# Kernel optimization log

Hardware: AMD Instinct MI355X
Metric: run time of the kernel (lower is better)

## Reference

```python
import jax, jax.numpy as jnp
import numpy as np

# seek_thermal sensor constants (hard-coded in the torch module)
HFOV, VFOV = 81.0, 59.0
H, W = 150, 200
P = 1024   # max_num_points
M = 5      # max_num_persons


def _cam_grids():
    fx = W / (2.0 * np.tan(np.deg2rad(HFOV) / 2.0))
    fy = H / (2.0 * np.tan(np.deg2rad(VFOV) / 2.0))
    x, y = np.meshgrid(np.arange(W), np.arange(H))
    x_cam = (x - W / 2.0) / fx
    y_cam = (y - H / 2.0) / fy
    return jnp.asarray(x_cam, jnp.float32), jnp.asarray(y_cam, jnp.float32)


def setup_inputs() -> dict:
    key = jax.random.key(0)
    k1, k2, k3 = jax.random.split(key, 3)
    B = 256
    depth = jax.random.uniform(k1, (B, H, W), jnp.float32, 0.0, 12.0)
    ind = jax.random.randint(k2, (B, H, W), 0, M + 1).astype(jnp.float32)
    extra = jax.random.normal(k3, (B, H, W), dtype=jnp.float32)
    return {"depth_mask_3C": jnp.stack([depth, ind, extra], axis=1)}


def _percentile(d_sorted, n, q):
    # np.percentile 'linear' interpolation on ascending sorted valid depths
    nf = n.astype(d_sorted.dtype)
    pos = q * jnp.maximum(nf - 1.0, 0.0)
    lo = jnp.floor(pos).astype(jnp.int32)
    hi = jnp.ceil(pos).astype(jnp.int32)
    frac = pos - lo.astype(d_sorted.dtype)
    return d_sorted[lo] * (1.0 - frac) + d_sorted[hi] * frac


def _person(depth, ind, x_cam, y_cam, p):
    # depth, ind: (H, W); p: scalar person id (float)
    mask = (ind == p) & (depth > 3.0)
    n = mask.sum()
    # invalid pixels pushed to +inf so the first n sorted entries are the valid depths
    d_sorted = jnp.sort(jnp.where(mask, depth, jnp.inf).reshape(-1))
    q1 = _percentile(d_sorted, n, 0.25)
    q3 = _percentile(d_sorted, n, 0.75)
    iqr = q3 - q1
    lb = q1 - 1.5 * iqr
    ub = q3 + 1.5 * iqr
    mask2 = (mask & (depth >= lb) & (depth <= ub)).reshape(-1)  # (H*W,)
    pts = jnp.stack(
        [(x_cam * depth).reshape(-1), (y_cam * depth).reshape(-1), depth.reshape(-1)],
        axis=-1,
    )  # (H*W, 3)
    # deterministic compaction: first max_num_points surviving pixels in raster order
    rank = jnp.cumsum(mask2.astype(jnp.int32)) - 1
    write_idx = jnp.where(mask2 & (rank < P), rank, P)  # slot P is a dump slot
    buf = jnp.zeros((P + 1, 3), depth.dtype).at[write_idx].set(
        jnp.where(mask2[:, None], pts, 0.0)
    )
    flag = mask2.any().astype(depth.dtype)
    flag_col = jnp.zeros((3,), depth.dtype).at[0].set(flag)
    return jnp.concatenate([buf[:P].T, flag_col[:, None]], axis=1)  # (3, P+1)


def reference(depth_mask_3C):
    x_cam, y_cam = _cam_grids()
    depth = depth_mask_3C[:, 0]
    ind = jnp.round(depth_mask_3C[:, 1])
    persons = jnp.arange(1, M + 1, dtype=depth.dtype)
    per_b = jax.vmap(_person, in_axes=(None, None, None, None, 0))
    res = jax.vmap(per_b, in_axes=(0, 0, None, None, None))(
        depth, ind, x_cam, y_cam, persons
    )  # (B, M, 3, P+1)
    B = depth.shape[0]
    return res.transpose(0, 2, 1, 3).reshape(B, 3, M * (P + 1))
```

## Files before the change

### kernel.cpp

```cpp
#include <hip/hip_runtime.h>
#include <math.h>

#define HW_N   30000
#define NV4    7500
#define W_IMG  200
#define H_IMG  150
#define NPERS  5
#define CAP    1024
#define NTHR   1024
#define NWAVE  16
#define CAPS   384
#define NREG   (NWAVE * NPERS)
#define BASE_BITS 0x40400000u

#ifndef M_PI
#define M_PI 3.14159265358979323846
#endif

__device__ __forceinline__ unsigned wave_incl_scan_u32(unsigned v, int lane) {
    #pragma unroll
    for (int d = 1; d < 64; d <<= 1) {
        unsigned t = __shfl_up(v, d, 64);
        if (lane >= d) v += t;
    }
    return v;
}

__device__ __forceinline__ void find_bucket(const unsigned* h, int nchunks, unsigned k,
                                            int lane, unsigned& bucket, unsigned& cl) {
    unsigned run = 0;
    bucket = 0; cl = 0;
    bool found = false;
    for (int c = 0; c < nchunks; ++c) {
        if (found) break;
        unsigned hv = h[c * 64 + lane] & 0xFFFFu;
        unsigned inc = wave_incl_scan_u32(hv, lane);
        unsigned tot = __shfl(inc, 63, 64);
        if (run + tot > k) {
            unsigned long long m = __ballot((run + inc) > k);
            int l = (int)__builtin_ctzll(m);
            bucket = (unsigned)(c * 64 + l);
            cl = run + __shfl(inc, l, 64) - __shfl(hv, l, 64);
            found = true;
        }
        run += tot;
    }
}

__device__ __forceinline__ int person_of(float f) {
    float r = rintf(f);
    int p = (int)r;
    return (p >= 1 && p <= NPERS && (float)p == r) ? p : 0;
}

extern "C" __global__ __launch_bounds__(NTHR)
void DepthMask2PointCloudFast_53472342835417_kernel(const float* __restrict__ in,
                                                    float* __restrict__ out) {
    const int b = blockIdx.x;
    const int tid = (int)threadIdx.x;
    const int lane = tid & 63;
    const int wv = tid >> 6;

    const float* __restrict__ depth = in + (size_t)b * 3u * HW_N;
    const float* __restrict__ indc = depth + HW_N;
    const float4* __restrict__ d4p = (const float4*)depth;
    const float4* __restrict__ i4p = (const float4*)indc;

    __shared__ unsigned s_vals[NREG * CAPS];
    __shared__ unsigned s_cur[NREG];
    __shared__ unsigned s_h1[NPERS * 256];
    __shared__ unsigned s_h2[20 * 256];
    __shared__ __align__(16) unsigned s_pref[24];
    __shared__ int      s_krem[20];
    __shared__ float    s_val[20];
    __shared__ unsigned s_n[NPERS];
    __shared__ float    s_lb[NPERS], s_ub[NPERS];
    __shared__ unsigned s_cnt[NWAVE][NPERS];
    __shared__ unsigned s_woff[NWAVE][NPERS];
    __shared__ unsigned s_tot[NPERS];
    __shared__ unsigned s_base[NPERS];
    __shared__ float    s_xc[W_IMG];
    __shared__ float    s_yc[H_IMG];

    for (int i = tid; i < NPERS * 256; i += NTHR) s_h1[i] = 0u;
    for (int i = tid; i < 20 * 256; i += NTHR) s_h2[i] = 0u;
    if (tid < NREG) s_cur[tid] = 0u;
    if (tid < NPERS) { s_base[tid] = 0u; s_tot[tid] = 0u; }
    if (tid < W_IMG) {
        const double fx = 200.0 / (2.0 * tan((81.0 * (M_PI / 180.0)) / 2.0));
        s_xc[tid] = (float)(((double)tid - 100.0) / fx);
    }
    {
        int ty = tid - 256;
        if (ty >= 0 && ty < H_IMG) {
            const double fy = 150.0 / (2.0 * tan((59.0 * (M_PI / 180.0)) / 2.0));
            s_yc[ty] = (float)(((double)ty - 75.0) / fy);
        }
    }
    __syncthreads();

    {
        int i = tid;
        float4 dd = d4p[i], ff = i4p[i];
        while (i < NV4) {
            int inx = i + NTHR;
            float4 dd2, ff2;
            if (inx < NV4) { dd2 = d4p[inx]; ff2 = i4p[inx]; }
            float de[4] = {dd.x, dd.y, dd.z, dd.w};
            float fe[4] = {ff.x, ff.y, ff.z, ff.w};
            #pragma unroll
            for (int e = 0; e < 4; ++e) {
                float d = de[e];
                int p = person_of(fe[e]);
                if (p && d > 3.0f) {
                    unsigned k24 = __float_as_uint(d) - BASE_BITS;
                    atomicAdd(&s_h1[(p - 1) * 256 + (k24 >> 16)], 1u);
                    int reg = wv * NPERS + (p - 1);
                    unsigned off = atomicAdd(&s_cur[reg], 1u);
                    if (off < CAPS) s_vals[reg * CAPS + off] = k24;
                }
            }
            dd = dd2; ff = ff2;
            i = inx;
        }
    }
    __syncthreads();

    if (tid < NPERS) {
        unsigned n = 0;
        for (int sh = 0; sh < NWAVE; ++sh) n += s_cur[sh * NPERS + tid];
        s_n[tid] = n;
    }
    __syncthreads();

    for (int q = wv; q < 20; q += NWAVE) {
        int p = q >> 2, s = q & 3;
        unsigned n = s_n[p];
        if (n == 0u) { if (lane == 0) s_pref[q] = 0xFFFFFFFFu; continue; }
        float nf = (float)n;
        float m1 = fmaxf(nf - 1.0f, 0.0f);
        float pos = ((s >> 1) ? 0.75f : 0.25f) * m1;
        unsigned k = (unsigned)((s & 1) ? (int)ceilf(pos) : (int)floorf(pos));
        unsigned bucket, cl;
        find_bucket(&s_h1[p * 256], 4, k, lane, bucket, cl);
        if (lane == 0) { s_pref[q] = bucket; s_krem[q] = (int)(k - cl); }
    }
    __syncthreads();

    for (int t = tid; t < NREG * CAPS; t += NTHR) {
        int reg = t / CAPS;
        int ii = t - reg * CAPS;
        unsigned cnt = s_cur[reg]; if (cnt > CAPS) cnt = CAPS;
        if ((unsigned)ii < cnt) {
            unsigned k24 = s_vals[t];
            int p = reg % NPERS;
            unsigned t8 = k24 >> 16;
            uint4 pr = *(const uint4*)&s_pref[p * 4];
            unsigned b8 = (k24 >> 8) & 255u;
            if (t8 == pr.x) atomicAdd(&s_h2[(p * 4 + 0) * 256 + b8], 1u);
            if (t8 == pr.y) atomicAdd(&s_h2[(p * 4 + 1) * 256 + b8], 1u);
            if (t8 == pr.z) atomicAdd(&s_h2[(p * 4 + 2) * 256 + b8], 1u);
            if (t8 == pr.w) atomicAdd(&s_h2[(p * 4 + 3) * 256 + b8], 1u);
        }
    }
    __syncthreads();

    for (int q = wv; q < 20; q += NWAVE) {
        int p = q >> 2;
        if (s_n[p] == 0u) continue;
        unsigned bucket, cl;
        find_bucket(&s_h2[q * 256], 4, (unsigned)s_krem[q], lane, bucket, cl);
        if (lane == 0) { s_pref[q] = (s_pref[q] << 8) | bucket; s_krem[q] -= (int)cl; }
    }
    __syncthreads();
    for (int i = tid; i < 20 * 256; i += NTHR) s_h2[i] = 0u;
    __syncthreads();

    for (int t = tid; t < NREG * CAPS; t += NTHR) {
        int reg = t / CAPS;
        int ii = t - reg * CAPS;
        unsigned cnt = s_cur[reg]; if (cnt > CAPS) cnt = CAPS;
        if ((unsigned)ii < cnt) {
            unsigned k24 = s_vals[t];
            int p = reg % NPERS;
            unsigned t16 = k24 >> 8;
            uint4 pr = *(const uint4*)&s_pref[p * 4];
            unsigned b8 = k24 & 255u;
            if (t16 == pr.x) atomicAdd(&s_h2[(p * 4 + 0) * 256 + b8], 1u);
            if (t16 == pr.y) atomicAdd(&s_h2[(p * 4 + 1) * 256 + b8], 1u);
            if (t16 == pr.z) atomicAdd(&s_h2[(p * 4 + 2) * 256 + b8], 1u);
            if (t16 == pr.w) atomicAdd(&s_h2[(p * 4 + 3) * 256 + b8], 1u);
        }
    }
    __syncthreads();

    for (int q = wv; q < 20; q += NWAVE) {
        int p = q >> 2;
        if (s_n[p] == 0u) continue;
        unsigned bucket, cl;
        find_bucket(&s_h2[q * 256], 4, (unsigned)s_krem[q], lane, bucket, cl);
        if (lane == 0) s_val[q] = __uint_as_float(BASE_BITS + ((s_pref[q] << 8) | bucket));
    }
    __syncthreads();

    if (tid < NPERS) {
        if (s_n[tid] == 0u) {
            s_lb[tid] = INFINITY; s_ub[tid] = -INFINITY;
        } else {
            float nf = (float)s_n[tid];
            float m1 = fmaxf(nf - 1.0f, 0.0f);
            float pos1 = 0.25f * m1, pos3 = 0.75f * m1;
            float fr1 = pos1 - floorf(pos1);
            float fr3 = pos3 - floorf(pos3);
            float q1 = __fadd_rn(__fmul_rn(s_val[tid * 4 + 0], __fsub_rn(1.0f, fr1)),
                                 __fmul_rn(s_val[tid * 4 + 1], fr1));
            float q3 = __fadd_rn(__fmul_rn(s_val[tid * 4 + 2], __fsub_rn(1.0f, fr3)),
                                 __fmul_rn(s_val[tid * 4 + 3], fr3));
            float iqr = __fsub_rn(q3, q1);
            float t15 = __fmul_rn(1.5f, iqr);
            s_lb[tid] = __fsub_rn(q1, t15);
            s_ub[tid] = __fadd_rn(q3, t15);
        }
    }
    __syncthreads();

    float* outb = out + (size_t)b * 3u * (NPERS * (CAP + 1));
    const int cstr = NPERS * (CAP + 1);

    for (int t0 = 0; t0 < NV4; t0 += NTHR) {
        int i = t0 + tid;
        int pf[4] = {0, 0, 0, 0};
        float dv[4] = {0.f, 0.f, 0.f, 0.f};
        if (i < NV4) {
            float4 dd = d4p[i];
            float4 ff = i4p[i];
            float de[4] = {dd.x, dd.y, dd.z, dd.w};
            float fe[4] = {ff.x, ff.y, ff.z, ff.w};
            #pragma unroll
            for (int e = 0; e < 4; ++e) {
                float d = de[e];
                int p = person_of(fe[e]);
                dv[e] = d;
                if (p && d > 3.0f && d >= s_lb[p - 1] && d <= s_ub[p - 1]) pf[e] = p;
            }
        }
        unsigned wexc[NPERS];
        #pragma unroll
        for (int pp = 0; pp < NPERS; ++pp) {
            unsigned c = (unsigned)((pf[0] == pp + 1) + (pf[1] == pp + 1) +
                                    (pf[2] == pp + 1) + (pf[3] == pp + 1));
            unsigned incl = wave_incl_scan_u32(c, lane);
            if (lane == 63) s_cnt[wv][pp] = incl;
            wexc[pp] = incl - c;
        }
        __syncthreads();
        if (tid < 16 * NPERS) {
            int p = tid >> 4, w = tid & 15;
            unsigned o = s_base[p];
            for (int w2 = 0; w2 < w; ++w2) o += s_cnt[w2][p];
            s_woff[w][p] = o;
            if (w == 15) s_tot[p] = o + s_cnt[15][p];
        }
        __syncthreads();
        #pragma unroll
        for (int pp = 0; pp < NPERS; ++pp) {
            unsigned m0 = (pf[0] == pp + 1), m1 = (pf[1] == pp + 1);
            unsigned m2 = (pf[2] == pp + 1), m3 = (pf[3] == pp + 1);
            if ((m0 | m1 | m2 | m3) != 0u) {
                unsigned basep = s_woff[wv][pp] + wexc[pp];
                #define WRITEPT(e, mm, pre)                                                \
                    if (mm) { unsigned off = basep + (pre);                                \
                        if (off < CAP) {                                                   \
                            int idx = i * 4 + e; int y = idx / W_IMG; int x = idx - y * W_IMG; \
                            size_t o = (size_t)pp * (CAP + 1) + off; float d = dv[e];      \
                            outb[o] = __fmul_rn(s_xc[x], d);                               \
                            outb[cstr + o] = __fmul_rn(s_yc[y], d);                        \
                            outb[2 * cstr + o] = d; } }
                WRITEPT(0, m0, 0u)
                WRITEPT(1, m1, m0)
                WRITEPT(2, m2, m0 + m1)
                WRITEPT(3, m3, m0 + m1 + m2)
                #undef WRITEPT
            }
        }
        if (tid < NPERS) s_base[tid] = s_tot[tid];
        bool done = true;
        #pragma unroll
        for (int pp = 0; pp < NPERS; ++pp) done = done && (s_tot[pp] >= (unsigned)CAP);
        if (done) break;
    }
    __syncthreads();

    for (int t = tid; t < NPERS * (CAP + 1); t += NTHR) {
        int p = t / (CAP + 1);
        int j = t - p * (CAP + 1);
        unsigned cnt = s_tot[p];
        size_t o = (size_t)p * (CAP + 1) + j;
        if (j == CAP) {
            outb[o] = (cnt > 0u) ? 1.0f : 0.0f;
            outb[cstr + o] = 0.0f;
            outb[2 * cstr + o] = 0.0f;
        } else if ((unsigned)j >= cnt) {
            outb[o] = 0.0f;
            outb[cstr + o] = 0.0f;
            outb[2 * cstr + o] = 0.0f;
        }
    }
}

extern "C" void kernel_launch(void* const* d_in, const int* in_sizes, int n_in,
                              void* d_out, int out_size, void* d_ws, size_t ws_size,
                              hipStream_t stream) {
    const float* in = (const float*)d_in[0];
    float* out = (float*)d_out;
    int B = in_sizes[0] / (3 * HW_N);
    hipLaunchKernelGGL(DepthMask2PointCloudFast_53472342835417_kernel,
                       dim3(B), dim3(NTHR), 0, stream, in, out);
}
```

Measured before the change: 52.95 us.

## Split per-image kernel into capture, select and output kernels via workspace

```diff
diff --git a/kernel.cpp b/kernel.cpp
--- a/kernel.cpp
+++ b/kernel.cpp
@@ -7,11 +7,8 @@
 #define H_IMG  150
 #define NPERS  5
 #define CAP    1024
-#define NTHR   1024
-#define NWAVE  16
-#define CAPS   384
-#define NREG   (NWAVE * NPERS)
 #define BASE_BITS 0x40400000u
+#define VCAP   4096
 
 #ifndef M_PI
 #define M_PI 3.14159265358979323846
@@ -26,8 +23,284 @@
     return v;
 }
 
-__device__ __forceinline__ void find_bucket(const unsigned* h, int nchunks, unsigned k,
-                                            int lane, unsigned& bucket, unsigned& cl) {
+__device__ __forceinline__ int person_of(float f) {
+    float r = rintf(f);
+    int p = (int)r;
+    return (p >= 1 && p <= NPERS && (float)p == r) ? p : 0;
+}
+
+__device__ __forceinline__ void sel256(const unsigned* h, unsigned k, int lane,
+                                       unsigned& bucket, unsigned& krem) {
+    unsigned run = 0; bucket = 0; krem = 0;
+    bool found = false;
+    #pragma unroll
+    for (int c = 0; c < 4; ++c) {
+        if (found) continue;
+        unsigned hv = h[c * 64 + lane];
+        unsigned inc = wave_incl_scan_u32(hv, lane);
+        unsigned tot = __shfl(inc, 63, 64);
+        if (run + tot > k) {
+            unsigned long long m = __ballot((run + inc) > k);
+            int l = (int)__builtin_ctzll(m);
+            bucket = (unsigned)(c * 64 + l);
+            krem = k - (run + __shfl(inc, l, 64) - __shfl(hv, l, 64));
+            found = true;
+        } else run += tot;
+    }
+}
+
+__global__ __launch_bounds__(256)
+void k1_capture(const float* __restrict__ in, unsigned* __restrict__ vals,
+                unsigned* __restrict__ cnt) {
+    const int bid = blockIdx.x;
+    const int b = bid >> 2, s = bid & 3;
+    const int tid = (int)threadIdx.x, lane = tid & 63;
+    const float* __restrict__ depth = in + (size_t)b * 3u * HW_N;
+    const float4* __restrict__ d4p = (const float4*)depth;
+    const float4* __restrict__ i4p = (const float4*)(depth + HW_N);
+    const int f40 = s * (NV4 / 4), f41 = f40 + (NV4 / 4);
+
+    for (int base4 = f40; base4 < f41; base4 += 256) {
+        int i = base4 + tid;
+        bool valid = i < f41;
+        float4 dd, ff;
+        if (valid) { dd = d4p[i]; ff = i4p[i]; }
+        int pf[4] = {0, 0, 0, 0};
+        unsigned kk[4] = {0, 0, 0, 0};
+        if (valid) {
+            float de[4] = {dd.x, dd.y, dd.z, dd.w};
+            float fe[4] = {ff.x, ff.y, ff.z, ff.w};
+            #pragma unroll
+            for (int e = 0; e < 4; ++e) {
+                float d = de[e];
+                int p = person_of(fe[e]);
+                if (p && d > 3.0f) { pf[e] = p; kk[e] = __float_as_uint(d) - BASE_BITS; }
+            }
+        }
+        #pragma unroll
+        for (int pp = 1; pp <= NPERS; ++pp) {
+            unsigned m0 = (pf[0] == pp), m1 = (pf[1] == pp);
+            unsigned m2 = (pf[2] == pp), m3 = (pf[3] == pp);
+            unsigned c = m0 + m1 + m2 + m3;
+            unsigned incl = wave_incl_scan_u32(c, lane);
+            unsigned tot = __shfl(incl, 63, 64);
+            if (tot == 0u) continue;
+            unsigned base = 0u;
+            if (lane == 0) base = atomicAdd(&cnt[b * NPERS + pp - 1], tot);
+            base = (unsigned)__shfl((int)base, 0, 64);
+            unsigned wexc = incl - c;
+            unsigned* vp = vals + (size_t)(b * NPERS + pp - 1) * VCAP;
+            unsigned o = base + wexc;
+            if (m0 && o < VCAP) vp[o] = kk[0];
+            o += m0;
+            if (m1 && o < VCAP) vp[o] = kk[1];
+            o += m1;
+            if (m2 && o < VCAP) vp[o] = kk[2];
+            o += m2;
+            if (m3 && o < VCAP) vp[o] = kk[3];
+        }
+    }
+}
+
+__global__ __launch_bounds__(256)
+void k2_select(const unsigned* __restrict__ vals, const unsigned* __restrict__ cnt,
+               float* __restrict__ bounds) {
+    const int bp = blockIdx.x;
+    const int tid = (int)threadIdx.x, lane = tid & 63, wv = tid >> 6;
+
+    __shared__ unsigned s_v[VCAP];
+    __shared__ unsigned s_h1[256];
+    __shared__ unsigned s_h2[4 * 256];
+    __shared__ unsigned s_pref[4];
+    __shared__ unsigned s_krem[4];
+    __shared__ float    s_val[4];
+
+    unsigned n = cnt[bp];
+    if (n == 0u) {
+        if (tid == 0) { bounds[bp * 2] = INFINITY; bounds[bp * 2 + 1] = -INFINITY; }
+        return;
+    }
+    unsigned nn = n > VCAP ? VCAP : n;
+    s_h1[tid] = 0u;
+    #pragma unroll
+    for (int j = 0; j < 4; ++j) s_h2[j * 256 + tid] = 0u;
+    __syncthreads();
+
+    const unsigned* vsrc = vals + (size_t)bp * VCAP;
+    for (int i = tid; i < (int)nn; i += 256) {
+        unsigned v = vsrc[i];
+        s_v[i] = v;
+        atomicAdd(&s_h1[v >> 16], 1u);
+    }
+    __syncthreads();
+
+    {
+        float nf = (float)n;
+        float m1 = fmaxf(nf - 1.0f, 0.0f);
+        float pos = ((wv >> 1) ? 0.75f : 0.25f) * m1;
+        unsigned k = (unsigned)((wv & 1) ? (int)ceilf(pos) : (int)floorf(pos));
+        unsigned bucket, krem;
+        sel256(s_h1, k, lane, bucket, krem);
+        if (lane == 0) { s_pref[wv] = bucket; s_krem[wv] = krem; }
+    }
+    __syncthreads();
+
+    {
+        unsigned p0 = s_pref[0], p1 = s_pref[1], p2 = s_pref[2], p3 = s_pref[3];
+        for (int i = tid; i < (int)nn; i += 256) {
+            unsigned v = s_v[i];
+            unsigned t8 = v >> 16, b8 = (v >> 8) & 255u;
+            if (t8 == p0) atomicAdd(&s_h2[b8], 1u);
+            if (t8 == p1) atomicAdd(&s_h2[256 + b8], 1u);
+            if (t8 == p2) atomicAdd(&s_h2[512 + b8], 1u);
+            if (t8 == p3) atomicAdd(&s_h2[768 + b8], 1u);
+        }
+    }
+    __syncthreads();
+    {
+        unsigned bucket, krem;
+        sel256(&s_h2[wv * 256], s_krem[wv], lane, bucket, krem);
+        if (lane == 0) { s_pref[wv] = (s_pref[wv] << 8) | bucket; s_krem[wv] = krem; }
+    }
+    __syncthreads();
+    #pragma unroll
+    for (int j = 0; j < 4; ++j) s_h2[j * 256 + tid] = 0u;
+    __syncthreads();
+
+    {
+        unsigned p0 = s_pref[0], p1 = s_pref[1], p2 = s_pref[2], p3 = s_pref[3];
+        for (int i = tid; i < (int)nn; i += 256) {
+            unsigned v = s_v[i];
+            unsigned t16 = v >> 8, b8 = v & 255u;
+            if (t16 == p0) atomicAdd(&s_h2[b8], 1u);
+            if (t16 == p1) atomicAdd(&s_h2[256 + b8], 1u);
+            if (t16 == p2) atomicAdd(&s_h2[512 + b8], 1u);
+            if (t16 == p3) atomicAdd(&s_h2[768 + b8], 1u);
+        }
+    }
+    __syncthreads();
+    {
+        unsigned bucket, krem;
+        sel256(&s_h2[wv * 256], s_krem[wv], lane, bucket, krem);
+        if (lane == 0) s_val[wv] = __uint_as_float(BASE_BITS + ((s_pref[wv] << 8) | bucket));
+    }
+    __syncthreads();
+
+    if (tid == 0) {
+        float nf = (float)n;
+        float m1 = fmaxf(nf - 1.0f, 0.0f);
+        float pos1 = 0.25f * m1, pos3 = 0.75f * m1;
+        float fr1 = pos1 - floorf(pos1);
+        float fr3 = pos3 - floorf(pos3);
+        float q1 = __fadd_rn(__fmul_rn(s_val[0], __fsub_rn(1.0f, fr1)),
+                             __fmul_rn(s_val[1], fr1));
+        float q3 = __fadd_rn(__fmul_rn(s_val[2], __fsub_rn(1.0f, fr3)),
+                             __fmul_rn(s_val[3], fr3));
+        float iqr = __fsub_rn(q3, q1);
+        float t15 = __fmul_rn(1.5f, iqr);
+        bounds[bp * 2]     = __fsub_rn(q1, t15);
+        bounds[bp * 2 + 1] = __fadd_rn(q3, t15);
+    }
+}
+
+__global__ __launch_bounds__(256)
+void k3_output(const float* __restrict__ in, const float* __restrict__ bounds,
+               float* __restrict__ out) {
+    const int bp = blockIdx.x;
+    const int b = bp / NPERS, p = bp % NPERS;
+    const int tid = (int)threadIdx.x, lane = tid & 63, wv = tid >> 6;
+    const int ptgt = p + 1;
+
+    __shared__ float s_xc[W_IMG], s_yc[H_IMG];
+    __shared__ unsigned s_wcnt[4], s_woff[4];
+    __shared__ unsigned s_gbase;
+
+    if (tid < W_IMG) {
+        const double fx = 200.0 / (2.0 * tan((81.0 * (M_PI / 180.0)) / 2.0));
+        s_xc[tid] = (float)(((double)tid - 100.0) / fx);
+    }
+    if (tid < H_IMG) {
+        const double fy = 150.0 / (2.0 * tan((59.0 * (M_PI / 180.0)) / 2.0));
+        s_yc[tid] = (float)(((double)tid - 75.0) / fy);
+    }
+    if (tid == 0) s_gbase = 0u;
+
+    const float lb = bounds[bp * 2], ub = bounds[bp * 2 + 1];
+    const float* __restrict__ depth = in + (size_t)b * 3u * HW_N;
+    const float4* __restrict__ d4p = (const float4*)depth;
+    const float4* __restrict__ i4p = (const float4*)(depth + HW_N);
+    float* r0 = out + (size_t)b * 3u * (NPERS * (CAP + 1)) + (size_t)p * (CAP + 1);
+    const int cstr = NPERS * (CAP + 1);
+    __syncthreads();
+
+    for (int base4 = 0; base4 < NV4; base4 += 256) {
+        int i = base4 + tid;
+        bool valid = i < NV4;
+        float4 dd, ff;
+        if (valid) { dd = d4p[i]; ff = i4p[i]; }
+        unsigned m[4] = {0, 0, 0, 0};
+        float dv[4] = {0.f, 0.f, 0.f, 0.f};
+        if (valid) {
+            float de[4] = {dd.x, dd.y, dd.z, dd.w};
+            float fe[4] = {ff.x, ff.y, ff.z, ff.w};
+            #pragma unroll
+            for (int e = 0; e < 4; ++e) {
+                float d = de[e];
+                dv[e] = d;
+                if (person_of(fe[e]) == ptgt && d > 3.0f && d >= lb && d <= ub) m[e] = 1u;
+            }
+        }
+        unsigned c = m[0] + m[1] + m[2] + m[3];
+        unsigned incl = wave_incl_scan_u32(c, lane);
+        if (lane == 63) s_wcnt[wv] = incl;
+        unsigned wexc = incl - c;
+        __syncthreads();
+        if (tid == 0) {
+            unsigned o = s_gbase;
+            #pragma unroll
+            for (int w = 0; w < 4; ++w) { s_woff[w] = o; o += s_wcnt[w]; }
+            s_gbase = o;
+        }
+        __syncthreads();
+        if (c) {
+            unsigned o = s_woff[wv] + wexc;
+            #pragma unroll
+            for (int e = 0; e < 4; ++e) {
+                if (m[e]) {
+                    if (o < CAP) {
+                        int idx = i * 4 + e;
+                        int y = idx / W_IMG, x = idx - y * W_IMG;
+                        float d = dv[e];
+                        r0[o]            = __fmul_rn(s_xc[x], d);
+                        r0[cstr + o]     = __fmul_rn(s_yc[y], d);
+                        r0[2 * cstr + o] = d;
+                    }
+                    ++o;
+                }
+            }
+        }
+        if (s_gbase >= (unsigned)CAP) break;
+    }
+    __syncthreads();
+    unsigned cntv = s_gbase;
+    unsigned cl = cntv > (unsigned)CAP ? (unsigned)CAP : cntv;
+    for (int j = (int)cl + tid; j < CAP; j += 256) {
+        r0[j] = 0.0f; r0[cstr + j] = 0.0f; r0[2 * cstr + j] = 0.0f;
+    }
+    if (tid == 0) {
+        r0[CAP] = (cntv > 0u) ? 1.0f : 0.0f;
+        r0[cstr + CAP] = 0.0f;
+        r0[2 * cstr + CAP] = 0.0f;
+    }
+}
+
+#define NTHR 1024
+#define NWAVE 16
+#define CAPS 384
+#define NREG (NWAVE * NPERS)
+
+__device__ __forceinline__ void find_bucket_fb(const unsigned* h, int nchunks, unsigned k,
+                                               int lane, unsigned& bucket, unsigned& cl) {
     unsigned run = 0;
     bucket = 0; cl = 0;
     bool found = false;
@@ -47,20 +320,12 @@
     }
 }
 
-__device__ __forceinline__ int person_of(float f) {
-    float r = rintf(f);
-    int p = (int)r;
-    return (p >= 1 && p <= NPERS && (float)p == r) ? p : 0;
-}
-
-extern "C" __global__ __launch_bounds__(NTHR)
-void DepthMask2PointCloudFast_53472342835417_kernel(const float* __restrict__ in,
-                                                    float* __restrict__ out) {
+__global__ __launch_bounds__(NTHR)
+void fb_kernel(const float* __restrict__ in, float* __restrict__ out) {
     const int b = blockIdx.x;
     const int tid = (int)threadIdx.x;
     const int lane = tid & 63;
     const int wv = tid >> 6;
-
     const float* __restrict__ depth = in + (size_t)b * 3u * HW_N;
     const float* __restrict__ indc = depth + HW_N;
     const float4* __restrict__ d4p = (const float4*)depth;
@@ -142,7 +407,7 @@
         float pos = ((s >> 1) ? 0.75f : 0.25f) * m1;
         unsigned k = (unsigned)((s & 1) ? (int)ceilf(pos) : (int)floorf(pos));
         unsigned bucket, cl;
-        find_bucket(&s_h1[p * 256], 4, k, lane, bucket, cl);
+        find_bucket_fb(&s_h1[p * 256], 4, k, lane, bucket, cl);
         if (lane == 0) { s_pref[q] = bucket; s_krem[q] = (int)(k - cl); }
     }
     __syncthreads();
@@ -169,7 +434,7 @@
         int p = q >> 2;
         if (s_n[p] == 0u) continue;
         unsigned bucket, cl;
-        find_bucket(&s_h2[q * 256], 4, (unsigned)s_krem[q], lane, bucket, cl);
+        find_bucket_fb(&s_h2[q * 256], 4, (unsigned)s_krem[q], lane, bucket, cl);
         if (lane == 0) { s_pref[q] = (s_pref[q] << 8) | bucket; s_krem[q] -= (int)cl; }
     }
     __syncthreads();
@@ -198,7 +463,7 @@
         int p = q >> 2;
         if (s_n[p] == 0u) continue;
         unsigned bucket, cl;
-        find_bucket(&s_h2[q * 256], 4, (unsigned)s_krem[q], lane, bucket, cl);
+        find_bucket_fb(&s_h2[q * 256], 4, (unsigned)s_krem[q], lane, bucket, cl);
         if (lane == 0) s_val[q] = __uint_as_float(BASE_BITS + ((s_pref[q] << 8) | bucket));
     }
     __syncthreads();
@@ -314,6 +579,23 @@
     const float* in = (const float*)d_in[0];
     float* out = (float*)d_out;
     int B = in_sizes[0] / (3 * HW_N);
-    hipLaunchKernelGGL(DepthMask2PointCloudFast_53472342835417_kernel,
-                       dim3(B), dim3(NTHR), 0, stream, in, out);
-}
+
+    const size_t vals_bytes = (size_t)B * NPERS * VCAP * 4;
+    const size_t cnt_off    = vals_bytes;
+    const size_t cnt_bytes  = (size_t)B * NPERS * 4;
+    const size_t bnd_off    = cnt_off + cnt_bytes;
+    const size_t bnd_bytes  = (size_t)B * NPERS * 2 * 4;
+    const size_t req        = bnd_off + bnd_bytes;
+
+    if (ws_size >= req) {
+        unsigned* vals = (unsigned*)d_ws;
+        unsigned* cnt  = (unsigned*)((char*)d_ws + cnt_off);
+        float* bounds  = (float*)((char*)d_ws + bnd_off);
+        hipMemsetAsync(cnt, 0, cnt_bytes, stream);
+        hipLaunchKernelGGL(k1_capture, dim3(B * 4), dim3(256), 0, stream, in, vals, cnt);
+        hipLaunchKernelGGL(k2_select, dim3(B * NPERS), dim3(256), 0, stream, vals, cnt, bounds);
+        hipLaunchKernelGGL(k3_output, dim3(B * NPERS), dim3(256), 0, stream, in, bounds, out);
+    } else {
+        hipLaunchKernelGGL(fb_kernel, dim3(B), dim3(NTHR), 0, stream, in, out);
+    }
+}
```

Measured after the change: 92.55 us. +74.8%, slower.

## Keep pixel indices in LDS buckets and compact from shared memory instead of rereading

Applied to the files above, without the earlier changes.

```diff
diff --git a/kernel.cpp b/kernel.cpp
--- a/kernel.cpp
+++ b/kernel.cpp
@@ -9,8 +9,7 @@
 #define CAP    1024
 #define NTHR   1024
 #define NWAVE  16
-#define CAPS   384
-#define NREG   (NWAVE * NPERS)
+#define WCAP   344
 #define BASE_BITS 0x40400000u
 
 #ifndef M_PI
@@ -26,24 +25,23 @@
     return v;
 }
 
-__device__ __forceinline__ void find_bucket(const unsigned* h, int nchunks, unsigned k,
-                                            int lane, unsigned& bucket, unsigned& cl) {
-    unsigned run = 0;
-    bucket = 0; cl = 0;
+__device__ __forceinline__ void find_bucket(const unsigned* h, int shift, unsigned k,
+                                            int lane, unsigned& bucket, unsigned& krem) {
+    unsigned run = 0; bucket = 0; krem = 0;
     bool found = false;
-    for (int c = 0; c < nchunks; ++c) {
-        if (found) break;
-        unsigned hv = h[c * 64 + lane] & 0xFFFFu;
+    #pragma unroll
+    for (int c = 0; c < 4; ++c) {
+        if (found) continue;
+        unsigned hv = (h[c * 64 + lane] >> shift) & 0xFFFFu;
         unsigned inc = wave_incl_scan_u32(hv, lane);
         unsigned tot = __shfl(inc, 63, 64);
         if (run + tot > k) {
             unsigned long long m = __ballot((run + inc) > k);
             int l = (int)__builtin_ctzll(m);
             bucket = (unsigned)(c * 64 + l);
-            cl = run + __shfl(inc, l, 64) - __shfl(hv, l, 64);
+            krem = k - (run + __shfl(inc, l, 64) - __shfl(hv, l, 64));
             found = true;
-        }
-        run += tot;
+        } else run += tot;
     }
 }
 
@@ -62,30 +60,27 @@
     const int wv = tid >> 6;
 
     const float* __restrict__ depth = in + (size_t)b * 3u * HW_N;
-    const float* __restrict__ indc = depth + HW_N;
     const float4* __restrict__ d4p = (const float4*)depth;
-    const float4* __restrict__ i4p = (const float4*)indc;
-
-    __shared__ unsigned s_vals[NREG * CAPS];
-    __shared__ unsigned s_cur[NREG];
+    const float4* __restrict__ i4p = (const float4*)(depth + HW_N);
+
+    __shared__ unsigned      sA[NPERS * NWAVE * WCAP];
+    __shared__ unsigned char sVb[NPERS * NWAVE * WCAP];
     __shared__ unsigned s_h1[NPERS * 256];
-    __shared__ unsigned s_h2[20 * 256];
-    __shared__ __align__(16) unsigned s_pref[24];
-    __shared__ int      s_krem[20];
+    __shared__ unsigned s_h2[10 * 256];
+    __shared__ unsigned s_rcnt[NPERS * NWAVE];
+    __shared__ unsigned s_pref[20];
+    __shared__ unsigned s_krem[20];
     __shared__ float    s_val[20];
     __shared__ unsigned s_n[NPERS];
     __shared__ float    s_lb[NPERS], s_ub[NPERS];
-    __shared__ unsigned s_cnt[NWAVE][NPERS];
-    __shared__ unsigned s_woff[NWAVE][NPERS];
+    __shared__ float    s_xc[W_IMG], s_yc[H_IMG];
+    __shared__ unsigned s_so[17];
+    __shared__ unsigned s_wc[NWAVE], s_wo[NWAVE];
+    __shared__ unsigned s_gb;
     __shared__ unsigned s_tot[NPERS];
-    __shared__ unsigned s_base[NPERS];
-    __shared__ float    s_xc[W_IMG];
-    __shared__ float    s_yc[H_IMG];
 
     for (int i = tid; i < NPERS * 256; i += NTHR) s_h1[i] = 0u;
-    for (int i = tid; i < 20 * 256; i += NTHR) s_h2[i] = 0u;
-    if (tid < NREG) s_cur[tid] = 0u;
-    if (tid < NPERS) { s_base[tid] = 0u; s_tot[tid] = 0u; }
+    for (int i = tid; i < 10 * 256; i += NTHR) s_h2[i] = 0u;
     if (tid < W_IMG) {
         const double fx = 200.0 / (2.0 * tan((81.0 * (M_PI / 180.0)) / 2.0));
         s_xc[tid] = (float)(((double)tid - 100.0) / fx);
@@ -100,39 +95,78 @@
     __syncthreads();
 
     {
-        int i = tid;
-        float4 dd = d4p[i], ff = i4p[i];
-        while (i < NV4) {
-            int inx = i + NTHR;
+        const int beg = (wv * NV4) / NWAVE;
+        const int end = ((wv + 1) * NV4) / NWAVE;
+        const unsigned long long lt = (lane == 0) ? 0ull : (~0ull >> (64 - lane));
+        unsigned cur[NPERS] = {0u, 0u, 0u, 0u, 0u};
+
+        int i0 = beg + lane;
+        float4 dd, ff;
+        if (i0 < end) { dd = d4p[i0]; ff = i4p[i0]; }
+        for (int t0 = beg; t0 < end; t0 += 64) {
+            int i = t0 + lane;
+            bool valid = i < end;
+            int inx = i + 64;
             float4 dd2, ff2;
-            if (inx < NV4) { dd2 = d4p[inx]; ff2 = i4p[inx]; }
-            float de[4] = {dd.x, dd.y, dd.z, dd.w};
-            float fe[4] = {ff.x, ff.y, ff.z, ff.w};
+            if (inx < end) { dd2 = d4p[inx]; ff2 = i4p[inx]; }
+
+            int pf[4] = {0, 0, 0, 0};
+            unsigned kk[4] = {0u, 0u, 0u, 0u};
+            if (valid) {
+                float de[4] = {dd.x, dd.y, dd.z, dd.w};
+                float fe[4] = {ff.x, ff.y, ff.z, ff.w};
+                #pragma unroll
+                for (int e = 0; e < 4; ++e) {
+                    int p = person_of(fe[e]);
+                    if (p && de[e] > 3.0f) {
+                        pf[e] = p;
+                        kk[e] = __float_as_uint(de[e]) - BASE_BITS;
+                        atomicAdd(&s_h1[(p - 1) * 256 + (kk[e] >> 16)], 1u);
+                    }
+                }
+            }
             #pragma unroll
-            for (int e = 0; e < 4; ++e) {
-                float d = de[e];
-                int p = person_of(fe[e]);
-                if (p && d > 3.0f) {
-                    unsigned k24 = __float_as_uint(d) - BASE_BITS;
-                    atomicAdd(&s_h1[(p - 1) * 256 + (k24 >> 16)], 1u);
-                    int reg = wv * NPERS + (p - 1);
-                    unsigned off = atomicAdd(&s_cur[reg], 1u);
-                    if (off < CAPS) s_vals[reg * CAPS + off] = k24;
+            for (int pp = 1; pp <= NPERS; ++pp) {
+                unsigned long long b0 = __ballot(pf[0] == pp);
+                unsigned long long b1 = __ballot(pf[1] == pp);
+                unsigned long long b2 = __ballot(pf[2] == pp);
+                unsigned long long b3 = __ballot(pf[3] == pp);
+                unsigned tot = (unsigned)(__popcll(b0) + __popcll(b1) +
+                                          __popcll(b2) + __popcll(b3));
+                if (tot == 0u) continue;
+                unsigned basel = (unsigned)(__popcll(b0 & lt) + __popcll(b1 & lt) +
+                                            __popcll(b2 & lt) + __popcll(b3 & lt));
+                unsigned o = cur[pp - 1] + basel;
+                unsigned rb = (unsigned)((pp - 1) * NWAVE + wv) * WCAP;
+                #pragma unroll
+                for (int e = 0; e < 4; ++e) {
+                    if (pf[e] == pp) {
+                        if (o < WCAP) {
+                            unsigned idx = (unsigned)(i * 4 + e);
+                            sA[rb + o]  = kk[e] | ((idx & 0xFFu) << 24);
+                            sVb[rb + o] = (unsigned char)(idx >> 8);
+                        }
+                        ++o;
+                    }
                 }
+                cur[pp - 1] += tot;
             }
             dd = dd2; ff = ff2;
-            i = inx;
+        }
+        if (lane == 0) {
+            #pragma unroll
+            for (int p = 0; p < NPERS; ++p)
+                s_rcnt[p * NWAVE + wv] = cur[p] > WCAP ? (unsigned)WCAP : cur[p];
         }
     }
     __syncthreads();
 
     if (tid < NPERS) {
         unsigned n = 0;
-        for (int sh = 0; sh < NWAVE; ++sh) n += s_cur[sh * NPERS + tid];
+        for (int w = 0; w < NWAVE; ++w) n += s_rcnt[tid * NWAVE + w];
         s_n[tid] = n;
     }
     __syncthreads();
-
     for (int q = wv; q < 20; q += NWAVE) {
         int p = q >> 2, s = q & 3;
         unsigned n = s_n[p];
@@ -141,64 +175,62 @@
         float m1 = fmaxf(nf - 1.0f, 0.0f);
         float pos = ((s >> 1) ? 0.75f : 0.25f) * m1;
         unsigned k = (unsigned)((s & 1) ? (int)ceilf(pos) : (int)floorf(pos));
-        unsigned bucket, cl;
-        find_bucket(&s_h1[p * 256], 4, k, lane, bucket, cl);
-        if (lane == 0) { s_pref[q] = bucket; s_krem[q] = (int)(k - cl); }
-    }
-    __syncthreads();
-
-    for (int t = tid; t < NREG * CAPS; t += NTHR) {
-        int reg = t / CAPS;
-        int ii = t - reg * CAPS;
-        unsigned cnt = s_cur[reg]; if (cnt > CAPS) cnt = CAPS;
-        if ((unsigned)ii < cnt) {
-            unsigned k24 = s_vals[t];
-            int p = reg % NPERS;
-            unsigned t8 = k24 >> 16;
-            uint4 pr = *(const uint4*)&s_pref[p * 4];
-            unsigned b8 = (k24 >> 8) & 255u;
-            if (t8 == pr.x) atomicAdd(&s_h2[(p * 4 + 0) * 256 + b8], 1u);
-            if (t8 == pr.y) atomicAdd(&s_h2[(p * 4 + 1) * 256 + b8], 1u);
-            if (t8 == pr.z) atomicAdd(&s_h2[(p * 4 + 2) * 256 + b8], 1u);
-            if (t8 == pr.w) atomicAdd(&s_h2[(p * 4 + 3) * 256 + b8], 1u);
-        }
-    }
-    __syncthreads();
-
+        unsigned bucket, krem;
+        find_bucket(&s_h1[p * 256], 0, k, lane, bucket, krem);
+        if (lane == 0) { s_pref[q] = bucket; s_krem[q] = krem; }
+    }
+    __syncthreads();
+
+    for (int t = tid; t < NPERS * NWAVE * WCAP; t += NTHR) {
+        int reg = t / WCAP;
+        int ii = t - reg * WCAP;
+        if ((unsigned)ii < s_rcnt[reg]) {
+            int p = reg >> 4;
+            unsigned key = sA[t] & 0x00FFFFFFu;
+            unsigned t8 = key >> 16, b8 = (key >> 8) & 255u;
+            unsigned a01 = (t8 == s_pref[p * 4 + 0] ? 1u : 0u) |
+                           (t8 == s_pref[p * 4 + 1] ? 0x10000u : 0u);
+            unsigned a23 = (t8 == s_pref[p * 4 + 2] ? 1u : 0u) |
+                           (t8 == s_pref[p * 4 + 3] ? 0x10000u : 0u);
+            if (a01) atomicAdd(&s_h2[(p * 2 + 0) * 256 + b8], a01);
+            if (a23) atomicAdd(&s_h2[(p * 2 + 1) * 256 + b8], a23);
+        }
+    }
+    __syncthreads();
     for (int q = wv; q < 20; q += NWAVE) {
-        int p = q >> 2;
+        int p = q >> 2, s = q & 3;
         if (s_n[p] == 0u) continue;
-        unsigned bucket, cl;
-        find_bucket(&s_h2[q * 256], 4, (unsigned)s_krem[q], lane, bucket, cl);
-        if (lane == 0) { s_pref[q] = (s_pref[q] << 8) | bucket; s_krem[q] -= (int)cl; }
-    }
-    __syncthreads();
-    for (int i = tid; i < 20 * 256; i += NTHR) s_h2[i] = 0u;
-    __syncthreads();
-
-    for (int t = tid; t < NREG * CAPS; t += NTHR) {
-        int reg = t / CAPS;
-        int ii = t - reg * CAPS;
-        unsigned cnt = s_cur[reg]; if (cnt > CAPS) cnt = CAPS;
-        if ((unsigned)ii < cnt) {
-            unsigned k24 = s_vals[t];
-            int p = reg % NPERS;
-            unsigned t16 = k24 >> 8;
-            uint4 pr = *(const uint4*)&s_pref[p * 4];
-            unsigned b8 = k24 & 255u;
-            if (t16 == pr.x) atomicAdd(&s_h2[(p * 4 + 0) * 256 + b8], 1u);
-            if (t16 == pr.y) atomicAdd(&s_h2[(p * 4 + 1) * 256 + b8], 1u);
-            if (t16 == pr.z) atomicAdd(&s_h2[(p * 4 + 2) * 256 + b8], 1u);
-            if (t16 == pr.w) atomicAdd(&s_h2[(p * 4 + 3) * 256 + b8], 1u);
-        }
-    }
-    __syncthreads();
-
+        unsigned bucket, krem;
+        find_bucket(&s_h2[(p * 2 + (s >> 1)) * 256], (s & 1) * 16, s_krem[q],
+                    lane, bucket, krem);
+        if (lane == 0) { s_pref[q] = (s_pref[q] << 8) | bucket; s_krem[q] = krem; }
+    }
+    __syncthreads();
+    for (int i = tid; i < 10 * 256; i += NTHR) s_h2[i] = 0u;
+    __syncthreads();
+
+    for (int t = tid; t < NPERS * NWAVE * WCAP; t += NTHR) {
+        int reg = t / WCAP;
+        int ii = t - reg * WCAP;
+        if ((unsigned)ii < s_rcnt[reg]) {
+            int p = reg >> 4;
+            unsigned key = sA[t] & 0x00FFFFFFu;
+            unsigned t16 = key >> 8, b8 = key & 255u;
+            unsigned a01 = (t16 == s_pref[p * 4 + 0] ? 1u : 0u) |
+                           (t16 == s_pref[p * 4 + 1] ? 0x10000u : 0u);
+            unsigned a23 = (t16 == s_pref[p * 4 + 2] ? 1u : 0u) |
+                           (t16 == s_pref[p * 4 + 3] ? 0x10000u : 0u);
+            if (a01) atomicAdd(&s_h2[(p * 2 + 0) * 256 + b8], a01);
+            if (a23) atomicAdd(&s_h2[(p * 2 + 1) * 256 + b8], a23);
+        }
+    }
+    __syncthreads();
     for (int q = wv; q < 20; q += NWAVE) {
-        int p = q >> 2;
+        int p = q >> 2, s = q & 3;
         if (s_n[p] == 0u) continue;
-        unsigned bucket, cl;
-        find_bucket(&s_h2[q * 256], 4, (unsigned)s_krem[q], lane, bucket, cl);
+        unsigned bucket, krem;
+        find_bucket(&s_h2[(p * 2 + (s >> 1)) * 256], (s & 1) * 16, s_krem[q],
+                    lane, bucket, krem);
         if (lane == 0) s_val[q] = __uint_as_float(BASE_BITS + ((s_pref[q] << 8) | bucket));
     }
     __syncthreads();
@@ -227,69 +259,59 @@
     float* outb = out + (size_t)b * 3u * (NPERS * (CAP + 1));
     const int cstr = NPERS * (CAP + 1);
 
-    for (int t0 = 0; t0 < NV4; t0 += NTHR) {
-        int i = t0 + tid;
-        int pf[4] = {0, 0, 0, 0};
-        float dv[4] = {0.f, 0.f, 0.f, 0.f};
-        if (i < NV4) {
-            float4 dd = d4p[i];
-            float4 ff = i4p[i];
-            float de[4] = {dd.x, dd.y, dd.z, dd.w};
-            float fe[4] = {ff.x, ff.y, ff.z, ff.w};
-            #pragma unroll
-            for (int e = 0; e < 4; ++e) {
-                float d = de[e];
-                int p = person_of(fe[e]);
-                dv[e] = d;
-                if (p && d > 3.0f && d >= s_lb[p - 1] && d <= s_ub[p - 1]) pf[e] = p;
-            }
-        }
-        unsigned wexc[NPERS];
-        #pragma unroll
-        for (int pp = 0; pp < NPERS; ++pp) {
-            unsigned c = (unsigned)((pf[0] == pp + 1) + (pf[1] == pp + 1) +
-                                    (pf[2] == pp + 1) + (pf[3] == pp + 1));
+    for (int p = 0; p < NPERS; ++p) {
+        if (tid == 0) {
+            unsigned o = 0;
+            for (int w = 0; w < NWAVE; ++w) { s_so[w] = o; o += s_rcnt[p * NWAVE + w]; }
+            s_so[NWAVE] = o;
+            s_gb = 0u;
+        }
+        __syncthreads();
+        const int np = (int)s_so[NWAVE];
+        const float lb = s_lb[p], ub = s_ub[p];
+        float* r0 = outb + (size_t)p * (CAP + 1);
+
+        for (int j0 = 0; j0 < np; j0 += NTHR) {
+            int j = j0 + tid;
+            bool pass = false;
+            float d = 0.0f;
+            unsigned idx = 0;
+            if (j < np) {
+                int w = 0;
+                #pragma unroll
+                for (int k2 = 1; k2 <= NWAVE; ++k2) w += (j >= (int)s_so[k2]) ? 1 : 0;
+                int t = (p * NWAVE + w) * WCAP + (j - (int)s_so[w]);
+                unsigned v = sA[t];
+                d = __uint_as_float((v & 0x00FFFFFFu) + BASE_BITS);
+                idx = (v >> 24) | ((unsigned)sVb[t] << 8);
+                pass = (d >= lb) && (d <= ub);
+            }
+            unsigned c = pass ? 1u : 0u;
             unsigned incl = wave_incl_scan_u32(c, lane);
-            if (lane == 63) s_cnt[wv][pp] = incl;
-            wexc[pp] = incl - c;
+            if (lane == 63) s_wc[wv] = incl;
+            __syncthreads();
+            if (tid == 0) {
+                unsigned o = s_gb;
+                #pragma unroll
+                for (int w = 0; w < NWAVE; ++w) { s_wo[w] = o; o += s_wc[w]; }
+                s_gb = o;
+            }
+            __syncthreads();
+            if (pass) {
+                unsigned o = s_wo[wv] + (incl - c);
+                if (o < CAP) {
+                    int y = (int)idx / W_IMG, x = (int)idx - y * W_IMG;
+                    r0[o]            = __fmul_rn(s_xc[x], d);
+                    r0[cstr + o]     = __fmul_rn(s_yc[y], d);
+                    r0[2 * cstr + o] = d;
+                }
+            }
+            if (s_gb >= (unsigned)CAP) break;
         }
         __syncthreads();
-        if (tid < 16 * NPERS) {
-            int p = tid >> 4, w = tid & 15;
-            unsigned o = s_base[p];
-            for (int w2 = 0; w2 < w; ++w2) o += s_cnt[w2][p];
-            s_woff[w][p] = o;
-            if (w == 15) s_tot[p] = o + s_cnt[15][p];
-        }
+        if (tid == 0) s_tot[p] = s_gb;
         __syncthreads();
-        #pragma unroll
-        for (int pp = 0; pp < NPERS; ++pp) {
-            unsigned m0 = (pf[0] == pp + 1), m1 = (pf[1] == pp + 1);
-            unsigned m2 = (pf[2] == pp + 1), m3 = (pf[3] == pp + 1);
-            if ((m0 | m1 | m2 | m3) != 0u) {
-                unsigned basep = s_woff[wv][pp] + wexc[pp];
-                #define WRITEPT(e, mm, pre)                                                \
-                    if (mm) { unsigned off = basep + (pre);                                \
-                        if (off < CAP) {                                                   \
-                            int idx = i * 4 + e; int y = idx / W_IMG; int x = idx - y * W_IMG; \
-                            size_t o = (size_t)pp * (CAP + 1) + off; float d = dv[e];      \
-                            outb[o] = __fmul_rn(s_xc[x], d);                               \
-                            outb[cstr + o] = __fmul_rn(s_yc[y], d);                        \
-                            outb[2 * cstr + o] = d; } }
-                WRITEPT(0, m0, 0u)
-                WRITEPT(1, m1, m0)
-                WRITEPT(2, m2, m0 + m1)
-                WRITEPT(3, m3, m0 + m1 + m2)
-                #undef WRITEPT
-            }
-        }
-        if (tid < NPERS) s_base[tid] = s_tot[tid];
-        bool done = true;
-        #pragma unroll
-        for (int pp = 0; pp < NPERS; ++pp) done = done && (s_tot[pp] >= (unsigned)CAP);
-        if (done) break;
-    }
-    __syncthreads();
+    }
 
     for (int t = tid; t < NPERS * (CAP + 1); t += NTHR) {
         int p = t / (CAP + 1);
@@ -297,12 +319,12 @@
         unsigned cnt = s_tot[p];
         size_t o = (size_t)p * (CAP + 1) + j;
         if (j == CAP) {
-            outb[o] = (cnt > 0u) ? 1.0f : 0.0f;
-            outb[cstr + o] = 0.0f;
+            outb[o]            = (cnt > 0u) ? 1.0f : 0.0f;
+            outb[cstr + o]     = 0.0f;
             outb[2 * cstr + o] = 0.0f;
-        } else if ((unsigned)j >= cnt) {
-            outb[o] = 0.0f;
-            outb[cstr + o] = 0.0f;
+        } else if ((unsigned)j >= (cnt > (unsigned)CAP ? (unsigned)CAP : cnt)) {
+            outb[o]            = 0.0f;
+            outb[cstr + o]     = 0.0f;
             outb[2 * cstr + o] = 0.0f;
         }
     }
```

After: 62.15 us. +17.4%, slower.
